# Kernel tuning notes

Hardware: AMD Instinct MI355X
Metric: run time of the kernel (lower is better)

The kernel has to match this reference:

```python
import jax, jax.numpy as jnp
import numpy as np

PATCH_SIZE = 128
NUM_HEADS = 16
DILATION = 1
POS_BND = int(0.8 * PATCH_SIZE * DILATION ** 0.5)  # 102
RPE_NUM = 2 * POS_BND + 1                            # 205
B, P = 256, PATCH_SIZE


def setup_inputs() -> dict:
    key = jax.random.key(0)
    k1, k2 = jax.random.split(key)
    # relative integer coordinates, roughly centered at 0 (clamped inside reference)
    xyz = jax.random.randint(k1, (B, P, P, 3), -150, 151, dtype=jnp.int32).astype(jnp.int64)
    # trunc_normal_(std=0.02) approximated by scaled normal
    rpe_table = jax.random.normal(k2, (3 * RPE_NUM, NUM_HEADS), dtype=jnp.float32) * 0.02
    return {"xyz": xyz, "rpe_table": rpe_table}


def reference(xyz, rpe_table):
    # idx: clamp coords, shift to [0, 2*pos_bnd], offset each axis into its table slice
    mul = jnp.arange(3, dtype=xyz.dtype) * RPE_NUM              # [3]
    idx = jnp.clip(xyz, -POS_BND, POS_BND) + POS_BND + mul      # [B,P,P,3]
    out = rpe_table[idx]                                        # [B,P,P,3,H] gather
    out = out.sum(axis=3)                                       # [B,P,P,H] sum over xyz axes
    return out.transpose(0, 3, 1, 2)                            # [B,H,P,P]
```

## Files before the change

### kernel.cpp

```cpp
#include <hip/hip_runtime.h>
#include <hip/hip_bf16.h>

#define P 128
#define NH 16
#define POS_BND 102
#define RPE_NUM 205
#define TROWS 615
#define HALF_OFF 2460
#define ROWS_PER_BLOCK 16

typedef float floatx4 __attribute__((ext_vector_type(4)));

__device__ __forceinline__ float blo(unsigned d) { return __uint_as_float(d << 16); }
__device__ __forceinline__ float bhi(unsigned d) { return __uint_as_float(d & 0xffff0000u); }
__device__ __forceinline__ unsigned pkbf(float a, float b) {
    unsigned r;
    asm("v_cvt_pk_bf16_f32 %0, %1, %2" : "=v"(r) : "v"(a), "v"(b));
    return r;
}

__global__ __launch_bounds__(256, 3)
void rpe_kernel(const int* __restrict__ xyz, const float* __restrict__ table,
                float* __restrict__ out) {
    __shared__ unsigned lt[2 * HALF_OFF];
    __shared__ unsigned su[4][NH][128];

    const int t = threadIdx.x;
    const int w = t >> 6, l = t & 63;

    for (int q = t; q < TROWS * 8; q += 256) {
        int row = q >> 3, d = q & 7;
        float2 v = reinterpret_cast<const float2*>(table)[row * 8 + d];
        unsigned a = (__float_as_uint(v.x) + 0x8000u) >> 16;
        unsigned b = (__float_as_uint(v.y) + 0x8000u) & 0xffff0000u;
        int dst = (d < 4) ? (row * 4 + d) : (HALF_OFF + row * 4 + (d - 4));
        lt[dst] = a | b;
    }

    const int r0 = blockIdx.x * ROWS_PER_BLOCK + 4 * w;
    const int2* xp = reinterpret_cast<const int2*>(xyz);

    int2 p0, p1, p2, p3, p4, p5;
    {
        size_t ba = (size_t)192 * r0 + 3 * l;
        size_t bb = (size_t)192 * (r0 + 1) + 3 * l;
        p0 = xp[ba]; p1 = xp[ba + 1]; p2 = xp[ba + 2];
        p3 = xp[bb]; p4 = xp[bb + 1]; p5 = xp[bb + 2];
    }
    __syncthreads();

    #pragma unroll
    for (int k = 0; k < 2; ++k) {
        const int ra = r0 + 2 * k;
        const int b  = ra >> 7;
        const int i  = ra & 127;

        int2 c0 = p0, c1 = p1, c2 = p2, c3 = p3, c4 = p4, c5 = p5;
        if (k == 0) {
            size_t ba = (size_t)192 * (r0 + 2) + 3 * l;
            size_t bb = (size_t)192 * (r0 + 3) + 3 * l;
            p0 = xp[ba]; p1 = xp[ba + 1]; p2 = xp[ba + 2];
            p3 = xp[bb]; p4 = xp[bb + 1]; p5 = xp[bb + 2];
        }

        #pragma unroll
        for (int s = 0; s < 2; ++s) {
            int x0, y0, z0, x1, y1, z1;
            if (s == 0) { x0 = c0.x; y0 = c0.y; z0 = c1.x; x1 = c1.y; y1 = c2.x; z1 = c2.y; }
            else        { x0 = c3.x; y0 = c3.y; z0 = c4.x; x1 = c4.y; y1 = c5.x; z1 = c5.y; }

            int t00 = min(max(x0, -POS_BND), POS_BND) + POS_BND;
            int t01 = min(max(y0, -POS_BND), POS_BND) + POS_BND + RPE_NUM;
            int t02 = min(max(z0, -POS_BND), POS_BND) + POS_BND + 2 * RPE_NUM;
            int t10 = min(max(x1, -POS_BND), POS_BND) + POS_BND;
            int t11 = min(max(y1, -POS_BND), POS_BND) + POS_BND + RPE_NUM;
            int t12 = min(max(z1, -POS_BND), POS_BND) + POS_BND + 2 * RPE_NUM;

            uint4 ga0 = *reinterpret_cast<const uint4*>(&lt[t00 * 4]);
            uint4 ga1 = *reinterpret_cast<const uint4*>(&lt[t01 * 4]);
            uint4 ga2 = *reinterpret_cast<const uint4*>(&lt[t02 * 4]);
            uint4 gb0 = *reinterpret_cast<const uint4*>(&lt[HALF_OFF + t00 * 4]);
            uint4 gb1 = *reinterpret_cast<const uint4*>(&lt[HALF_OFF + t01 * 4]);
            uint4 gb2 = *reinterpret_cast<const uint4*>(&lt[HALF_OFF + t02 * 4]);
            uint4 gc0 = *reinterpret_cast<const uint4*>(&lt[t10 * 4]);
            uint4 gc1 = *reinterpret_cast<const uint4*>(&lt[t11 * 4]);
            uint4 gc2 = *reinterpret_cast<const uint4*>(&lt[t12 * 4]);
            uint4 gd0 = *reinterpret_cast<const uint4*>(&lt[HALF_OFF + t10 * 4]);
            uint4 gd1 = *reinterpret_cast<const uint4*>(&lt[HALF_OFF + t11 * 4]);
            uint4 gd2 = *reinterpret_cast<const uint4*>(&lt[HALF_OFF + t12 * 4]);

            unsigned* srow = &su[w][0][s * 64 + l];
            srow[ 0*128] = pkbf(blo(ga0.x)+blo(ga1.x)+blo(ga2.x), blo(gc0.x)+blo(gc1.x)+blo(gc2.x));
            srow[ 1*128] = pkbf(bhi(ga0.x)+bhi(ga1.x)+bhi(ga2.x), bhi(gc0.x)+bhi(gc1.x)+bhi(gc2.x));
            srow[ 2*128] = pkbf(blo(ga0.y)+blo(ga1.y)+blo(ga2.y), blo(gc0.y)+blo(gc1.y)+blo(gc2.y));
            srow[ 3*128] = pkbf(bhi(ga0.y)+bhi(ga1.y)+bhi(ga2.y), bhi(gc0.y)+bhi(gc1.y)+bhi(gc2.y));
            srow[ 4*128] = pkbf(blo(ga0.z)+blo(ga1.z)+blo(ga2.z), blo(gc0.z)+blo(gc1.z)+blo(gc2.z));
            srow[ 5*128] = pkbf(bhi(ga0.z)+bhi(ga1.z)+bhi(ga2.z), bhi(gc0.z)+bhi(gc1.z)+bhi(gc2.z));
            srow[ 6*128] = pkbf(blo(ga0.w)+blo(ga1.w)+blo(ga2.w), blo(gc0.w)+blo(gc1.w)+blo(gc2.w));
            srow[ 7*128] = pkbf(bhi(ga0.w)+bhi(ga1.w)+bhi(ga2.w), bhi(gc0.w)+bhi(gc1.w)+bhi(gc2.w));
            srow[ 8*128] = pkbf(blo(gb0.x)+blo(gb1.x)+blo(gb2.x), blo(gd0.x)+blo(gd1.x)+blo(gd2.x));
            srow[ 9*128] = pkbf(bhi(gb0.x)+bhi(gb1.x)+bhi(gb2.x), bhi(gd0.x)+bhi(gd1.x)+bhi(gd2.x));
            srow[10*128] = pkbf(blo(gb0.y)+blo(gb1.y)+blo(gb2.y), blo(gd0.y)+blo(gd1.y)+blo(gd2.y));
            srow[11*128] = pkbf(bhi(gb0.y)+bhi(gb1.y)+bhi(gb2.y), bhi(gd0.y)+bhi(gd1.y)+bhi(gd2.y));
            srow[12*128] = pkbf(blo(gb0.z)+blo(gb1.z)+blo(gb2.z), blo(gd0.z)+blo(gd1.z)+blo(gd2.z));
            srow[13*128] = pkbf(bhi(gb0.z)+bhi(gb1.z)+bhi(gb2.z), bhi(gd0.z)+bhi(gd1.z)+bhi(gd2.z));
            srow[14*128] = pkbf(blo(gb0.w)+blo(gb1.w)+blo(gb2.w), blo(gd0.w)+blo(gd1.w)+blo(gd2.w));
            srow[15*128] = pkbf(bhi(gb0.w)+bhi(gb1.w)+bhi(gb2.w), bhi(gd0.w)+bhi(gd1.w)+bhi(gd2.w));
        }

        const size_t pbase = ((size_t)b * NH) * (P * P) + (size_t)i * P + 4 * l;
        #pragma unroll
        for (int h = 0; h < NH; ++h) {
            uint2 v = *reinterpret_cast<const uint2*>(&su[w][h][2 * l]);
            floatx4 f = { blo(v.x), bhi(v.x), blo(v.y), bhi(v.y) };
            __builtin_nontemporal_store(f,
                reinterpret_cast<floatx4*>(out + pbase + (size_t)h * (P * P)));
        }
    }
}

extern "C" void kernel_launch(void* const* d_in, const int* in_sizes, int n_in,
                              void* d_out, int out_size, void* d_ws, size_t ws_size,
                              hipStream_t stream) {
    const int*   xyz   = (const int*)d_in[0];
    const float* table = (const float*)d_in[1];
    float*       out   = (float*)d_out;

    const int total_rows = 256 * P;
    const int grid = total_rows / ROWS_PER_BLOCK;
    rpe_kernel<<<grid, 256, 0, stream>>>(xyz, table, out);
}
```

Before: 54.89 us.

## Split heads across wave pairs to halve per-wave registers and LDS staging

Each pair of waves now shares a group of 8 rows, with each wave computing only one half (8 heads) of the bf16 table. This halves per-wave gathers, registers and the shared staging buffer, and launch bounds are raised to allow 4 blocks per SM. The aim is higher occupancy to better hide store latency in this write-bound kernel. In exchange, xyz coordinates are loaded twice (once per wave of a pair) and each wave loops over more rows.

```diff
diff --git a/kernel.cpp b/kernel.cpp
--- a/kernel.cpp
+++ b/kernel.cpp
@@ -19,11 +19,11 @@
     return r;
 }
 
-__global__ __launch_bounds__(256, 3)
+__global__ __launch_bounds__(256, 4)
 void rpe_kernel(const int* __restrict__ xyz, const float* __restrict__ table,
                 float* __restrict__ out) {
     __shared__ unsigned lt[2 * HALF_OFF];
-    __shared__ unsigned su[4][NH][128];
+    __shared__ unsigned su[4][8][128];
 
     const int t = threadIdx.x;
     const int w = t >> 6, l = t & 63;
@@ -37,7 +37,10 @@
         lt[dst] = a | b;
     }
 
-    const int r0 = blockIdx.x * ROWS_PER_BLOCK + 4 * w;
+    const int pair = w >> 1;
+    const int hsel = w & 1;
+    const int hoff = hsel ? HALF_OFF : 0;
+    const int r0 = blockIdx.x * ROWS_PER_BLOCK + pair * 8;
     const int2* xp = reinterpret_cast<const int2*>(xyz);
 
     int2 p0, p1, p2, p3, p4, p5;
@@ -50,15 +53,15 @@
     __syncthreads();
 
     #pragma unroll
-    for (int k = 0; k < 2; ++k) {
+    for (int k = 0; k < 4; ++k) {
         const int ra = r0 + 2 * k;
         const int b  = ra >> 7;
         const int i  = ra & 127;
 
         int2 c0 = p0, c1 = p1, c2 = p2, c3 = p3, c4 = p4, c5 = p5;
-        if (k == 0) {
-            size_t ba = (size_t)192 * (r0 + 2) + 3 * l;
-            size_t bb = (size_t)192 * (r0 + 3) + 3 * l;
+        if (k < 3) {
+            size_t ba = (size_t)192 * (ra + 2) + 3 * l;
+            size_t bb = (size_t)192 * (ra + 3) + 3 * l;
             p0 = xp[ba]; p1 = xp[ba + 1]; p2 = xp[ba + 2];
             p3 = xp[bb]; p4 = xp[bb + 1]; p5 = xp[bb + 2];
         }
@@ -69,52 +72,38 @@
             if (s == 0) { x0 = c0.x; y0 = c0.y; z0 = c1.x; x1 = c1.y; y1 = c2.x; z1 = c2.y; }
             else        { x0 = c3.x; y0 = c3.y; z0 = c4.x; x1 = c4.y; y1 = c5.x; z1 = c5.y; }
 
-            int t00 = min(max(x0, -POS_BND), POS_BND) + POS_BND;
-            int t01 = min(max(y0, -POS_BND), POS_BND) + POS_BND + RPE_NUM;
-            int t02 = min(max(z0, -POS_BND), POS_BND) + POS_BND + 2 * RPE_NUM;
-            int t10 = min(max(x1, -POS_BND), POS_BND) + POS_BND;
-            int t11 = min(max(y1, -POS_BND), POS_BND) + POS_BND + RPE_NUM;
-            int t12 = min(max(z1, -POS_BND), POS_BND) + POS_BND + 2 * RPE_NUM;
+            const int t00 = min(max(x0, -POS_BND), POS_BND) + POS_BND;
+            const int t01 = min(max(y0, -POS_BND), POS_BND) + POS_BND + RPE_NUM;
+            const int t02 = min(max(z0, -POS_BND), POS_BND) + POS_BND + 2 * RPE_NUM;
+            const int t10 = min(max(x1, -POS_BND), POS_BND) + POS_BND;
+            const int t11 = min(max(y1, -POS_BND), POS_BND) + POS_BND + RPE_NUM;
+            const int t12 = min(max(z1, -POS_BND), POS_BND) + POS_BND + 2 * RPE_NUM;
 
-            uint4 ga0 = *reinterpret_cast<const uint4*>(&lt[t00 * 4]);
-            uint4 ga1 = *reinterpret_cast<const uint4*>(&lt[t01 * 4]);
-            uint4 ga2 = *reinterpret_cast<const uint4*>(&lt[t02 * 4]);
-            uint4 gb0 = *reinterpret_cast<const uint4*>(&lt[HALF_OFF + t00 * 4]);
-            uint4 gb1 = *reinterpret_cast<const uint4*>(&lt[HALF_OFF + t01 * 4]);
-            uint4 gb2 = *reinterpret_cast<const uint4*>(&lt[HALF_OFF + t02 * 4]);
-            uint4 gc0 = *reinterpret_cast<const uint4*>(&lt[t10 * 4]);
-            uint4 gc1 = *reinterpret_cast<const uint4*>(&lt[t11 * 4]);
-            uint4 gc2 = *reinterpret_cast<const uint4*>(&lt[t12 * 4]);
-            uint4 gd0 = *reinterpret_cast<const uint4*>(&lt[HALF_OFF + t10 * 4]);
-            uint4 gd1 = *reinterpret_cast<const uint4*>(&lt[HALF_OFF + t11 * 4]);
-            uint4 gd2 = *reinterpret_cast<const uint4*>(&lt[HALF_OFF + t12 * 4]);
+            uint4 ga0 = *reinterpret_cast<const uint4*>(&lt[hoff + t00 * 4]);
+            uint4 ga1 = *reinterpret_cast<const uint4*>(&lt[hoff + t01 * 4]);
+            uint4 ga2 = *reinterpret_cast<const uint4*>(&lt[hoff + t02 * 4]);
+            uint4 gc0 = *reinterpret_cast<const uint4*>(&lt[hoff + t10 * 4]);
+            uint4 gc1 = *reinterpret_cast<const uint4*>(&lt[hoff + t11 * 4]);
+            uint4 gc2 = *reinterpret_cast<const uint4*>(&lt[hoff + t12 * 4]);
 
             unsigned* srow = &su[w][0][s * 64 + l];
-            srow[ 0*128] = pkbf(blo(ga0.x)+blo(ga1.x)+blo(ga2.x), blo(gc0.x)+blo(gc1.x)+blo(gc2.x));
-            srow[ 1*128] = pkbf(bhi(ga0.x)+bhi(ga1.x)+bhi(ga2.x), bhi(gc0.x)+bhi(gc1.x)+bhi(gc2.x));
-            srow[ 2*128] = pkbf(blo(ga0.y)+blo(ga1.y)+blo(ga2.y), blo(gc0.y)+blo(gc1.y)+blo(gc2.y));
-            srow[ 3*128] = pkbf(bhi(ga0.y)+bhi(ga1.y)+bhi(ga2.y), bhi(gc0.y)+bhi(gc1.y)+bhi(gc2.y));
-            srow[ 4*128] = pkbf(blo(ga0.z)+blo(ga1.z)+blo(ga2.z), blo(gc0.z)+blo(gc1.z)+blo(gc2.z));
-            srow[ 5*128] = pkbf(bhi(ga0.z)+bhi(ga1.z)+bhi(ga2.z), bhi(gc0.z)+bhi(gc1.z)+bhi(gc2.z));
-            srow[ 6*128] = pkbf(blo(ga0.w)+blo(ga1.w)+blo(ga2.w), blo(gc0.w)+blo(gc1.w)+blo(gc2.w));
-            srow[ 7*128] = pkbf(bhi(ga0.w)+bhi(ga1.w)+bhi(ga2.w), bhi(gc0.w)+bhi(gc1.w)+bhi(gc2.w));
-            srow[ 8*128] = pkbf(blo(gb0.x)+blo(gb1.x)+blo(gb2.x), blo(gd0.x)+blo(gd1.x)+blo(gd2.x));
-            srow[ 9*128] = pkbf(bhi(gb0.x)+bhi(gb1.x)+bhi(gb2.x), bhi(gd0.x)+bhi(gd1.x)+bhi(gd2.x));
-            srow[10*128] = pkbf(blo(gb0.y)+blo(gb1.y)+blo(gb2.y), blo(gd0.y)+blo(gd1.y)+blo(gd2.y));
-            srow[11*128] = pkbf(bhi(gb0.y)+bhi(gb1.y)+bhi(gb2.y), bhi(gd0.y)+bhi(gd1.y)+bhi(gd2.y));
-            srow[12*128] = pkbf(blo(gb0.z)+blo(gb1.z)+blo(gb2.z), blo(gd0.z)+blo(gd1.z)+blo(gd2.z));
-            srow[13*128] = pkbf(bhi(gb0.z)+bhi(gb1.z)+bhi(gb2.z), bhi(gd0.z)+bhi(gd1.z)+bhi(gd2.z));
-            srow[14*128] = pkbf(blo(gb0.w)+blo(gb1.w)+blo(gb2.w), blo(gd0.w)+blo(gd1.w)+blo(gd2.w));
-            srow[15*128] = pkbf(bhi(gb0.w)+bhi(gb1.w)+bhi(gb2.w), bhi(gd0.w)+bhi(gd1.w)+bhi(gd2.w));
+            srow[0*128] = pkbf(blo(ga0.x)+blo(ga1.x)+blo(ga2.x), blo(gc0.x)+blo(gc1.x)+blo(gc2.x));
+            srow[1*128] = pkbf(bhi(ga0.x)+bhi(ga1.x)+bhi(ga2.x), bhi(gc0.x)+bhi(gc1.x)+bhi(gc2.x));
+            srow[2*128] = pkbf(blo(ga0.y)+blo(ga1.y)+blo(ga2.y), blo(gc0.y)+blo(gc1.y)+blo(gc2.y));
+            srow[3*128] = pkbf(bhi(ga0.y)+bhi(ga1.y)+bhi(ga2.y), bhi(gc0.y)+bhi(gc1.y)+bhi(gc2.y));
+            srow[4*128] = pkbf(blo(ga0.z)+blo(ga1.z)+blo(ga2.z), blo(gc0.z)+blo(gc1.z)+blo(gc2.z));
+            srow[5*128] = pkbf(bhi(ga0.z)+bhi(ga1.z)+bhi(ga2.z), bhi(gc0.z)+bhi(gc1.z)+bhi(gc2.z));
+            srow[6*128] = pkbf(blo(ga0.w)+blo(ga1.w)+blo(ga2.w), blo(gc0.w)+blo(gc1.w)+blo(gc2.w));
+            srow[7*128] = pkbf(bhi(ga0.w)+bhi(ga1.w)+bhi(ga2.w), bhi(gc0.w)+bhi(gc1.w)+bhi(gc2.w));
         }
 
-        const size_t pbase = ((size_t)b * NH) * (P * P) + (size_t)i * P + 4 * l;
+        const size_t rbase = ((size_t)(b * NH + hsel * 8)) * (P * P) + (size_t)i * P + 4 * l;
         #pragma unroll
-        for (int h = 0; h < NH; ++h) {
+        for (int h = 0; h < 8; ++h) {
             uint2 v = *reinterpret_cast<const uint2*>(&su[w][h][2 * l]);
             floatx4 f = { blo(v.x), bhi(v.x), blo(v.y), bhi(v.y) };
             __builtin_nontemporal_store(f,
-                reinterpret_cast<floatx4*>(out + pbase + (size_t)h * (P * P)));
+                reinterpret_cast<floatx4*>(out + rbase + (size_t)h * (P * P)));
         }
     }
 }
```

Result: no change. 55.79 us (+1.6%).
